# Kernel tuning notes

Hardware: AMD Instinct MI355X
Metric: run time of the kernel (lower is better)

Reference implementation:

```python
import jax, jax.numpy as jnp
import numpy as np

N, F_IN, H1, NHEADS, H2, H3 = 4096, 512, 128, 4, 256, 64
ALPHA = 0.2
NEG = -9e15


def setup_inputs() -> dict:
    key = jax.random.key(0)
    k_x, k_adj, k_watt, k_a, k_w1, k_w2 = jax.random.split(key, 6)
    x = jax.random.normal(k_x, (N, F_IN), dtype=jnp.float32)
    adj = (jax.random.uniform(k_adj, (N, N)) < 0.004).astype(jnp.float32)
    adj = adj.at[jnp.arange(N), jnp.arange(N)].set(1.0)
    # xavier-ish init scales
    W_att = jax.random.normal(k_watt, (NHEADS, F_IN, H1), dtype=jnp.float32) * (1.0 / np.sqrt(F_IN))
    a = jax.random.normal(k_a, (NHEADS, 2 * H1), dtype=jnp.float32) * 0.1
    W1 = jax.random.normal(k_w1, (NHEADS * H1, H2), dtype=jnp.float32) * (1.0 / np.sqrt(NHEADS * H1))
    W2 = jax.random.normal(k_w2, (H2, H3), dtype=jnp.float32) * (1.0 / np.sqrt(H2))
    return {"x": x, "adj": adj, "W_att": W_att, "a": a, "W1": W1, "W2": W2}


def reference(x, adj, W_att, a, W1, W2):
    h1 = W_att.shape[-1]
    # --- multi-head GAT (dense masked attention, faithful to source) ---
    Wh = jnp.einsum('nf,hfo->hno', x, W_att)              # [H, N, h1]
    a1, a2 = a[:, :h1], a[:, h1:]                          # each [H, h1]
    s1 = jnp.einsum('hno,ho->hn', Wh, a1)                  # [H, N]
    s2 = jnp.einsum('hno,ho->hn', Wh, a2)                  # [H, N]
    e = jax.nn.leaky_relu(s1[:, :, None] + s2[:, None, :], ALPHA)  # [H, N, N]
    att = jax.nn.softmax(jnp.where(adj[None] > 0, e, NEG), axis=-1)
    h = jnp.einsum('hnm,hmo->hno', att, Wh)                # [H, N, h1]
    xcat = jnp.transpose(h, (1, 0, 2)).reshape(x.shape[0], -1)  # [N, H*h1]
    xr = jax.nn.relu(xcat)
    # --- GCN layers: support = x @ W; out = adj @ support ---
    g1 = jax.nn.relu(adj @ (xr @ W1))                      # [N, H2]
    g2 = adj @ (g1 @ W2)                                   # [N, H3]
    return g2, jax.nn.softmax(g2, axis=1)
```

## Files before the change

kernel.cpp:

```cpp
#include <hip/hip_runtime.h>
#include <hip/hip_bf16.h>

#define NN    4096
#define FIN   512
#define NH1   128
#define NH    4
#define NH2   256
#define NH3   64
#define CAP   64
#define ALPHA 0.2f

typedef float f32x4 __attribute__((ext_vector_type(4)));
typedef __bf16 bf16x8 __attribute__((ext_vector_type(8)));

__device__ __forceinline__ unsigned short f2bf(float f) {
    union { float f; unsigned u; } x; x.f = f;
    unsigned r = x.u + 0x7fff + ((x.u >> 16) & 1);
    return (unsigned short)(r >> 16);
}
__device__ __forceinline__ float bf2f(ushort u) {
    union { unsigned u; float f; } x; x.u = ((unsigned)u) << 16;
    return x.f;
}
__device__ __forceinline__ float bflo(unsigned w) {
    union { unsigned u; float f; } x; x.u = w << 16; return x.f;
}
__device__ __forceinline__ float bfhi(unsigned w) {
    union { unsigned u; float f; } x; x.u = w & 0xffff0000u; return x.f;
}

#define C_X     2048
#define C_WATT  (C_X + 1024)
#define C_W1T   (C_WATT + 512)
#define C_W2B   (C_W1T + 16)
#define C_Z     (C_W2B + 32)

__global__ __launch_bounds__(256) void k_conv(
    const float* __restrict__ x, ushort* __restrict__ xb,
    const float* __restrict__ W_att, ushort* __restrict__ Wattb,
    const float* __restrict__ W1, ushort* __restrict__ W1t,
    const float* __restrict__ W2, ushort* __restrict__ W2b,
    float* __restrict__ s1s2) {
    int bid = blockIdx.x;
    int tid = threadIdx.x;
    if (bid < C_X) {
        int i = (bid * 256 + tid) * 4;
        float4 v = *reinterpret_cast<const float4*>(x + i);
        ushort4 o;
        o.x = f2bf(v.x); o.y = f2bf(v.y); o.z = f2bf(v.z); o.w = f2bf(v.w);
        *reinterpret_cast<ushort4*>(xb + i) = o;
    } else if (bid < C_WATT) {
        int idx = (bid - C_X) * 256 + tid;
        int col = idx >> 9, f = idx & 511;
        int h = col >> 7, o = col & 127;
        Wattb[idx] = f2bf(W_att[h * (FIN * NH1) + f * NH1 + o]);
    } else if (bid < C_W1T) {
        int idx = (bid - C_WATT) * 256 + tid;
        int c = idx >> 9, r = idx & 511;
        W1t[idx] = f2bf(W1[(size_t)r * NH2 + c]);
    } else if (bid < C_W2B) {
        int i = ((bid - C_W1T) * 256 + tid) * 4;
        float4 v = *reinterpret_cast<const float4*>(W2 + i);
        ushort4 o;
        o.x = f2bf(v.x); o.y = f2bf(v.y); o.z = f2bf(v.z); o.w = f2bf(v.w);
        *reinterpret_cast<ushort4*>(W2b + i) = o;
    } else {
        int i = (bid - C_W2B) * 256 + tid;
        f32x4 z = {0.f, 0.f, 0.f, 0.f};
        *reinterpret_cast<f32x4*>(s1s2 + i * 4) = z;
    }
}

#define GBM 64
#define GBN 64
#define GBK 64
template <int SCORES>
__global__ __launch_bounds__(256) void k_gemm_bf16(const ushort* __restrict__ A,
                                                   const ushort* __restrict__ Bt,
                                                   ushort* __restrict__ Cb,
                                                   const float* __restrict__ av,
                                                   float* __restrict__ s1,
                                                   float* __restrict__ s2,
                                                   int M, int N, int K) {
    __shared__ ushort As[2][GBM * GBK];
    __shared__ ushort Bs[2][GBN * GBK];
    const int tid = threadIdx.x;
    const int wid = tid >> 6;
    const int lane = tid & 63;
    const int row0 = blockIdx.y * GBM;
    const int col0 = blockIdx.x * GBN;
    const int wr = wid >> 1, wc = wid & 1;

    f32x4 acc[2][2] = {};
    const int nt = K / GBK;

    auto stage = [&](int buf, int k0) {
        #pragma unroll
        for (int j = 0; j < 2; ++j) {
            int ci = j * 256 + tid;
            int r = ci >> 3;
            int sc = (ci & 7) ^ (r & 7);
            const ushort* ga = A + (size_t)(row0 + r) * K + k0 + sc * 8;
            const ushort* gb = Bt + (size_t)(col0 + r) * K + k0 + sc * 8;
            ushort* la = &As[buf][(j * 256 + wid * 64) * 8];
            ushort* lb = &Bs[buf][(j * 256 + wid * 64) * 8];
            __builtin_amdgcn_global_load_lds(
                (const __attribute__((address_space(1))) unsigned int*)ga,
                (__attribute__((address_space(3))) unsigned int*)la, 16, 0, 0);
            __builtin_amdgcn_global_load_lds(
                (const __attribute__((address_space(1))) unsigned int*)gb,
                (__attribute__((address_space(3))) unsigned int*)lb, 16, 0, 0);
        }
    };

    stage(0, 0);
    __syncthreads();
    int cur = 0;
    for (int t = 0; t < nt; ++t) {
        if (t + 1 < nt) stage(cur ^ 1, (t + 1) * GBK);
        #pragma unroll
        for (int kk = 0; kk < 2; ++kk) {
            bf16x8 af[2], bfv[2];
            #pragma unroll
            for (int m = 0; m < 2; ++m) {
                int r = wr * 32 + m * 16 + (lane & 15);
                int kc = kk * 4 + (lane >> 4);
                int off = r * GBK + (((kc ^ (r & 7)) & 7) << 3);
                af[m] = *reinterpret_cast<const bf16x8*>(&As[cur][off]);
            }
            #pragma unroll
            for (int n = 0; n < 2; ++n) {
                int c = wc * 32 + n * 16 + (lane & 15);
                int kc = kk * 4 + (lane >> 4);
                int off = c * GBK + (((kc ^ (c & 7)) & 7) << 3);
                bfv[n] = *reinterpret_cast<const bf16x8*>(&Bs[cur][off]);
            }
            #pragma unroll
            for (int m = 0; m < 2; ++m)
                #pragma unroll
                for (int n = 0; n < 2; ++n)
                    acc[m][n] = __builtin_amdgcn_mfma_f32_16x16x32_bf16(af[m], bfv[n], acc[m][n], 0, 0, 0);
        }
        __syncthreads();
        cur ^= 1;
    }
    #pragma unroll
    for (int m = 0; m < 2; ++m)
        #pragma unroll
        for (int n = 0; n < 2; ++n) {
            int col = col0 + wc * 32 + n * 16 + (lane & 15);
            #pragma unroll
            for (int j2 = 0; j2 < 4; ++j2) {
                int row = row0 + wr * 32 + m * 16 + (lane >> 4) * 4 + j2;
                Cb[(size_t)row * N + col] = f2bf(acc[m][n][j2]);
            }
        }
    if (SCORES) {
        int h = col0 >> 7;
        float a1v[2], a2v[2];
        #pragma unroll
        for (int n = 0; n < 2; ++n) {
            int colh = (col0 & 127) + wc * 32 + n * 16 + (lane & 15);
            a1v[n] = av[h * 256 + colh];
            a2v[n] = av[h * 256 + 128 + colh];
        }
        #pragma unroll
        for (int m = 0; m < 2; ++m)
            #pragma unroll
            for (int j2 = 0; j2 < 4; ++j2) {
                float v1 = acc[m][0][j2] * a1v[0] + acc[m][1][j2] * a1v[1];
                float v2 = acc[m][0][j2] * a2v[0] + acc[m][1][j2] * a2v[1];
                #pragma unroll
                for (int off = 1; off < 16; off <<= 1) {
                    v1 += __shfl_xor(v1, off);
                    v2 += __shfl_xor(v2, off);
                }
                if ((lane & 15) == 0) {
                    int row = row0 + wr * 32 + m * 16 + (lane >> 4) * 4 + j2;
                    atomicAdd(&s1[h * NN + row], v1);
                    atomicAdd(&s2[h * NN + row], v2);
                }
            }
    }
}

__global__ __launch_bounds__(256) void k_attn_csr(const float* __restrict__ adj,
                                                  const ushort* __restrict__ Whb,
                                                  const float* __restrict__ s1,
                                                  const float* __restrict__ s2,
                                                  int* __restrict__ nbr,
                                                  int* __restrict__ cnt,
                                                  ushort* __restrict__ xrb) {
    __shared__ int lds_list[4][64];
    __shared__ int lds_cnt[4];
    __shared__ int mlist[CAP];
    __shared__ int stot;
    int n = blockIdx.x;
    int tid = threadIdx.x;
    int wid = tid >> 6;
    int lane = tid & 63;

    const uint4* arow = (const uint4*)(adj + (size_t)n * NN);
    uint4 v[4];
    #pragma unroll
    for (int it = 0; it < 4; ++it) v[it] = arow[wid * 256 + it * 64 + lane];
    const unsigned long long below = (1ull << lane) - 1ull;
    int base = 0;
    #pragma unroll
    for (int it = 0; it < 4; ++it) {
        unsigned long long b0 = __ballot(v[it].x != 0u);
        unsigned long long b1 = __ballot(v[it].y != 0u);
        unsigned long long b2 = __ballot(v[it].z != 0u);
        unsigned long long b3 = __ballot(v[it].w != 0u);
        int pre = __popcll(b0 & below) + __popcll(b1 & below) +
                  __popcll(b2 & below) + __popcll(b3 & below);
        int col0 = wid * 1024 + it * 256 + lane * 4;
        int pos = base + pre;
        if (v[it].x != 0u) { if (pos < 64) lds_list[wid][pos] = col0;     ++pos; }
        if (v[it].y != 0u) { if (pos < 64) lds_list[wid][pos] = col0 + 1; ++pos; }
        if (v[it].z != 0u) { if (pos < 64) lds_list[wid][pos] = col0 + 2; ++pos; }
        if (v[it].w != 0u) { if (pos < 64) lds_list[wid][pos] = col0 + 3; ++pos; }
        base += __popcll(b0) + __popcll(b1) + __popcll(b2) + __popcll(b3);
    }
    if (lane == 0) lds_cnt[wid] = base;
    __syncthreads();
    int c0 = lds_cnt[0], c1 = lds_cnt[1], c2 = lds_cnt[2], c3 = lds_cnt[3];
    {
        int off = (wid > 0 ? c0 : 0) + (wid > 1 ? c1 : 0) + (wid > 2 ? c2 : 0);
        int my = lds_cnt[wid]; if (my > 64) my = 64;
        if (lane < my) {
            int gpos = off + lane;
            if (gpos < CAP) {
                mlist[gpos] = lds_list[wid][lane];
                nbr[n * CAP + gpos] = lds_list[wid][lane];
            }
        }
        if (tid == 0) {
            int tot = c0 + c1 + c2 + c3;
            stot = tot < CAP ? tot : CAP;
            cnt[n] = stot;
        }
    }
    __syncthreads();
    int c = stot;

    int h = wid;
    int m = mlist[lane < c ? lane : 0];
    float e = -1e30f;
    float s1n = s1[h * NN + n];
    if (lane < c) {
        float t = s1n + s2[h * NN + m];
        e = (t >= 0.0f) ? t : ALPHA * t;
    }
    float mx = e;
    #pragma unroll
    for (int off = 32; off; off >>= 1) mx = fmaxf(mx, __shfl_xor(mx, off));
    float p = (lane < c) ? __expf(e - mx) : 0.0f;
    float s = p;
    #pragma unroll
    for (int off = 32; off; off >>= 1) s += __shfl_xor(s, off);
    p /= s;
    const ushort* wb = Whb + h * 128 + 2 * lane;
    float acc0 = 0.0f, acc1 = 0.0f;
    int cp4 = (c + 3) & ~3;
    for (int j = 0; j < cp4; j += 4) {
        float p0 = __shfl(p, j),     p1 = __shfl(p, j + 1);
        float p2 = __shfl(p, j + 2), p3 = __shfl(p, j + 3);
        int   m0 = __shfl(m, j),     m1 = __shfl(m, j + 1);
        int   m2 = __shfl(m, j + 2), m3 = __shfl(m, j + 3);
        unsigned w0 = *reinterpret_cast<const unsigned*>(wb + (size_t)m0 * 512);
        unsigned w1 = *reinterpret_cast<const unsigned*>(wb + (size_t)m1 * 512);
        unsigned w2 = *reinterpret_cast<const unsigned*>(wb + (size_t)m2 * 512);
        unsigned w3 = *reinterpret_cast<const unsigned*>(wb + (size_t)m3 * 512);
        acc0 = fmaf(p0, bflo(w0), acc0); acc1 = fmaf(p0, bfhi(w0), acc1);
        acc0 = fmaf(p1, bflo(w1), acc0); acc1 = fmaf(p1, bfhi(w1), acc1);
        acc0 = fmaf(p2, bflo(w2), acc0); acc1 = fmaf(p2, bfhi(w2), acc1);
        acc0 = fmaf(p3, bflo(w3), acc0); acc1 = fmaf(p3, bfhi(w3), acc1);
    }
    unsigned ow = (unsigned)f2bf(fmaxf(acc0, 0.0f)) | ((unsigned)f2bf(fmaxf(acc1, 0.0f)) << 16);
    *reinterpret_cast<unsigned*>(xrb + (size_t)n * 512 + h * 128 + 2 * lane) = ow;
}

__global__ __launch_bounds__(256) void k_g1y2(const ushort* __restrict__ y1b,
                                              const int* __restrict__ nbr,
                                              const int* __restrict__ cnt,
                                              const ushort* __restrict__ W2b,
                                              float* __restrict__ y2) {
    __shared__ float g1s[NH2];
    __shared__ float part[4][NH3];
    int n = blockIdx.x;
    int tid = threadIdx.x;
    int c = cnt[n];
    const int* nb = nbr + n * CAP;
    if (tid < 128) {
        float acc0 = 0.0f, acc1 = 0.0f;
        const ushort* yb = y1b + 2 * tid;
        for (int j = 0; j < c; j += 4) {
            int i0 = nb[j];
            int i1 = nb[(j + 1 < c) ? j + 1 : j];
            int i2 = nb[(j + 2 < c) ? j + 2 : j];
            int i3 = nb[(j + 3 < c) ? j + 3 : j];
            float f1 = (j + 1 < c) ? 1.f : 0.f;
            float f2 = (j + 2 < c) ? 1.f : 0.f;
            float f3 = (j + 3 < c) ? 1.f : 0.f;
            unsigned w0 = *reinterpret_cast<const unsigned*>(yb + (size_t)i0 * NH2);
            unsigned w1 = *reinterpret_cast<const unsigned*>(yb + (size_t)i1 * NH2);
            unsigned w2 = *reinterpret_cast<const unsigned*>(yb + (size_t)i2 * NH2);
            unsigned w3 = *reinterpret_cast<const unsigned*>(yb + (size_t)i3 * NH2);
            acc0 += bflo(w0); acc1 += bfhi(w0);
            acc0 = fmaf(f1, bflo(w1), acc0); acc1 = fmaf(f1, bfhi(w1), acc1);
            acc0 = fmaf(f2, bflo(w2), acc0); acc1 = fmaf(f2, bfhi(w2), acc1);
            acc0 = fmaf(f3, bflo(w3), acc0); acc1 = fmaf(f3, bfhi(w3), acc1);
        }
        g1s[2 * tid]     = fmaxf(acc0, 0.0f);
        g1s[2 * tid + 1] = fmaxf(acc1, 0.0f);
    }
    __syncthreads();
    int q = tid >> 6, col = tid & 63;
    float acc = 0.0f;
    #pragma unroll 8
    for (int i = 0; i < 64; ++i) {
        int k = q * 64 + i;
        acc = fmaf(g1s[k], bf2f(W2b[k * NH3 + col]), acc);
    }
    part[q][col] = acc;
    __syncthreads();
    if (tid < 64)
        y2[(size_t)n * NH3 + tid] = part[0][tid] + part[1][tid] + part[2][tid] + part[3][tid];
}

__global__ void k_final(const float* __restrict__ Y2, const int* __restrict__ nbr,
                        const int* __restrict__ cnt, float* __restrict__ out) {
    int n = blockIdx.x;
    int lane = threadIdx.x;
    int c = cnt[n];
    const int* nb = nbr + n * CAP;
    float acc = 0.0f;
    for (int j = 0; j < c; j += 4) {
        int i0 = nb[j];
        int i1 = nb[(j + 1 < c) ? j + 1 : j];
        int i2 = nb[(j + 2 < c) ? j + 2 : j];
        int i3 = nb[(j + 3 < c) ? j + 3 : j];
        float f1 = (j + 1 < c) ? 1.f : 0.f;
        float f2 = (j + 2 < c) ? 1.f : 0.f;
        float f3 = (j + 3 < c) ? 1.f : 0.f;
        float v0 = Y2[(size_t)i0 * NH3 + lane];
        float v1 = Y2[(size_t)i1 * NH3 + lane];
        float v2 = Y2[(size_t)i2 * NH3 + lane];
        float v3 = Y2[(size_t)i3 * NH3 + lane];
        acc += v0;
        acc = fmaf(f1, v1, acc);
        acc = fmaf(f2, v2, acc);
        acc = fmaf(f3, v3, acc);
    }
    out[(size_t)n * NH3 + lane] = acc;
    float mx = acc;
    #pragma unroll
    for (int off = 32; off; off >>= 1) mx = fmaxf(mx, __shfl_xor(mx, off));
    float p = __expf(acc - mx);
    float s = p;
    #pragma unroll
    for (int off = 32; off; off >>= 1) s += __shfl_xor(s, off);
    out[(size_t)NN * NH3 + (size_t)n * NH3 + lane] = p / s;
}

extern "C" void kernel_launch(void* const* d_in, const int* in_sizes, int n_in,
                              void* d_out, int out_size, void* d_ws, size_t ws_size,
                              hipStream_t stream) {
    const float* x     = (const float*)d_in[0];
    const float* adj   = (const float*)d_in[1];
    const float* W_att = (const float*)d_in[2];
    const float* a     = (const float*)d_in[3];
    const float* W1    = (const float*)d_in[4];
    const float* W2    = (const float*)d_in[5];
    float* out = (float*)d_out;

    char* p = (char*)d_ws;
    ushort* xb    = (ushort*)p; p += (size_t)NN * FIN * 2;
    ushort* Wattb = (ushort*)p; p += (size_t)FIN * NH * NH1 * 2;
    ushort* W1t   = (ushort*)p; p += (size_t)NH2 * (NH * NH1) * 2;
    ushort* W2b   = (ushort*)p; p += (size_t)NH2 * NH3 * 2;
    ushort* Whb   = (ushort*)p; p += (size_t)NN * NH * NH1 * 2;
    float*  s1    = (float*)p;  p += (size_t)NH * NN * 4;
    float*  s2    = (float*)p;  p += (size_t)NH * NN * 4;
    int*    nbr   = (int*)p;    p += (size_t)NN * CAP * 4;
    int*    cnt   = (int*)p;    p += (size_t)NN * 4;
    ushort* xrb   = (ushort*)p; p += (size_t)NN * NH * NH1 * 2;
    ushort* y1b   = (ushort*)p; p += (size_t)NN * NH2 * 2;
    float*  y2    = (float*)p;  p += (size_t)NN * NH3 * 4;

    k_conv<<<C_Z, 256, 0, stream>>>(x, xb, W_att, Wattb, W1, W1t, W2, W2b, s1);
    k_gemm_bf16<1><<<dim3((NH * NH1) / GBN, NN / GBM), 256, 0, stream>>>(
        xb, Wattb, Whb, a, s1, s2, NN, NH * NH1, FIN);
    k_attn_csr<<<NN, 256, 0, stream>>>(adj, Whb, s1, s2, nbr, cnt, xrb);
    k_gemm_bf16<0><<<dim3(NH2 / GBN, NN / GBM), 256, 0, stream>>>(
        xrb, W1t, y1b, nullptr, nullptr, nullptr, NN, NH2, NH * NH1);
    k_g1y2<<<NN, 256, 0, stream>>>(y1b, nbr, cnt, W2b, y2);
    k_final<<<NN, 64, 0, stream>>>(y2, nbr, cnt, out);
}
```

Measured before the change: 70.73 us.

## Template GEMM row tile, unroll gather loops by eight, pack four rows per final block

Result: faster. 67.50 us (-4.6%).

```diff
diff --git a/kernel.cpp b/kernel.cpp
--- a/kernel.cpp
+++ b/kernel.cpp
@@ -71,42 +71,45 @@
     }
 }
 
-#define GBM 64
-#define GBN 64
-#define GBK 64
-template <int SCORES>
-__global__ __launch_bounds__(256) void k_gemm_bf16(const ushort* __restrict__ A,
-                                                   const ushort* __restrict__ Bt,
-                                                   ushort* __restrict__ Cb,
-                                                   const float* __restrict__ av,
-                                                   float* __restrict__ s1,
-                                                   float* __restrict__ s2,
-                                                   int M, int N, int K) {
-    __shared__ ushort As[2][GBM * GBK];
-    __shared__ ushort Bs[2][GBN * GBK];
+template <int SCORES, int MT>
+__global__ __launch_bounds__(256) void k_gemm(const ushort* __restrict__ A,
+                                              const ushort* __restrict__ Bt,
+                                              ushort* __restrict__ Cb,
+                                              const float* __restrict__ av,
+                                              float* __restrict__ s1,
+                                              float* __restrict__ s2,
+                                              int M, int N, int K) {
+    __shared__ ushort As[2][32 * MT * 64];
+    __shared__ ushort Bs[2][64 * 64];
     const int tid = threadIdx.x;
     const int wid = tid >> 6;
     const int lane = tid & 63;
-    const int row0 = blockIdx.y * GBM;
-    const int col0 = blockIdx.x * GBN;
+    const int row0 = blockIdx.y * (32 * MT);
+    const int col0 = blockIdx.x * 64;
     const int wr = wid >> 1, wc = wid & 1;
 
-    f32x4 acc[2][2] = {};
-    const int nt = K / GBK;
+    f32x4 acc[MT][2] = {};
+    const int nt = K / 64;
 
     auto stage = [&](int buf, int k0) {
+        #pragma unroll
+        for (int j = 0; j < MT; ++j) {
+            int ci = j * 256 + tid;
+            int r = ci >> 3;
+            int sc = (ci & 7) ^ (r & 7);
+            const ushort* ga = A + (size_t)(row0 + r) * K + k0 + sc * 8;
+            ushort* la = &As[buf][(size_t)ci * 8];
+            __builtin_amdgcn_global_load_lds(
+                (const __attribute__((address_space(1))) unsigned int*)ga,
+                (__attribute__((address_space(3))) unsigned int*)la, 16, 0, 0);
+        }
         #pragma unroll
         for (int j = 0; j < 2; ++j) {
             int ci = j * 256 + tid;
             int r = ci >> 3;
             int sc = (ci & 7) ^ (r & 7);
-            const ushort* ga = A + (size_t)(row0 + r) * K + k0 + sc * 8;
             const ushort* gb = Bt + (size_t)(col0 + r) * K + k0 + sc * 8;
-            ushort* la = &As[buf][(j * 256 + wid * 64) * 8];
-            ushort* lb = &Bs[buf][(j * 256 + wid * 64) * 8];
-            __builtin_amdgcn_global_load_lds(
-                (const __attribute__((address_space(1))) unsigned int*)ga,
-                (__attribute__((address_space(3))) unsigned int*)la, 16, 0, 0);
+            ushort* lb = &Bs[buf][(size_t)ci * 8];
             __builtin_amdgcn_global_load_lds(
                 (const __attribute__((address_space(1))) unsigned int*)gb,
                 (__attribute__((address_space(3))) unsigned int*)lb, 16, 0, 0);
@@ -117,26 +120,26 @@
     __syncthreads();
     int cur = 0;
     for (int t = 0; t < nt; ++t) {
-        if (t + 1 < nt) stage(cur ^ 1, (t + 1) * GBK);
+        if (t + 1 < nt) stage(cur ^ 1, (t + 1) * 64);
         #pragma unroll
         for (int kk = 0; kk < 2; ++kk) {
-            bf16x8 af[2], bfv[2];
-            #pragma unroll
-            for (int m = 0; m < 2; ++m) {
-                int r = wr * 32 + m * 16 + (lane & 15);
+            bf16x8 af[MT], bfv[2];
+            #pragma unroll
+            for (int m = 0; m < MT; ++m) {
+                int r = wr * (16 * MT) + m * 16 + (lane & 15);
                 int kc = kk * 4 + (lane >> 4);
-                int off = r * GBK + (((kc ^ (r & 7)) & 7) << 3);
+                int off = r * 64 + (((kc ^ (r & 7)) & 7) << 3);
                 af[m] = *reinterpret_cast<const bf16x8*>(&As[cur][off]);
             }
             #pragma unroll
             for (int n = 0; n < 2; ++n) {
                 int c = wc * 32 + n * 16 + (lane & 15);
                 int kc = kk * 4 + (lane >> 4);
-                int off = c * GBK + (((kc ^ (c & 7)) & 7) << 3);
+                int off = c * 64 + (((kc ^ (c & 7)) & 7) << 3);
                 bfv[n] = *reinterpret_cast<const bf16x8*>(&Bs[cur][off]);
             }
             #pragma unroll
-            for (int m = 0; m < 2; ++m)
+            for (int m = 0; m < MT; ++m)
                 #pragma unroll
                 for (int n = 0; n < 2; ++n)
                     acc[m][n] = __builtin_amdgcn_mfma_f32_16x16x32_bf16(af[m], bfv[n], acc[m][n], 0, 0, 0);
@@ -145,13 +148,13 @@
         cur ^= 1;
     }
     #pragma unroll
-    for (int m = 0; m < 2; ++m)
+    for (int m = 0; m < MT; ++m)
         #pragma unroll
         for (int n = 0; n < 2; ++n) {
             int col = col0 + wc * 32 + n * 16 + (lane & 15);
             #pragma unroll
             for (int j2 = 0; j2 < 4; ++j2) {
-                int row = row0 + wr * 32 + m * 16 + (lane >> 4) * 4 + j2;
+                int row = row0 + wr * (16 * MT) + m * 16 + (lane >> 4) * 4 + j2;
                 Cb[(size_t)row * N + col] = f2bf(acc[m][n][j2]);
             }
         }
@@ -165,7 +168,7 @@
             a2v[n] = av[h * 256 + 128 + colh];
         }
         #pragma unroll
-        for (int m = 0; m < 2; ++m)
+        for (int m = 0; m < MT; ++m)
             #pragma unroll
             for (int j2 = 0; j2 < 4; ++j2) {
                 float v1 = acc[m][0][j2] * a1v[0] + acc[m][1][j2] * a1v[1];
@@ -176,7 +179,7 @@
                     v2 += __shfl_xor(v2, off);
                 }
                 if ((lane & 15) == 0) {
-                    int row = row0 + wr * 32 + m * 16 + (lane >> 4) * 4 + j2;
+                    int row = row0 + wr * (16 * MT) + m * 16 + (lane >> 4) * 4 + j2;
                     atomicAdd(&s1[h * NN + row], v1);
                     atomicAdd(&s2[h * NN + row], v2);
                 }
@@ -262,20 +265,22 @@
     p /= s;
     const ushort* wb = Whb + h * 128 + 2 * lane;
     float acc0 = 0.0f, acc1 = 0.0f;
-    int cp4 = (c + 3) & ~3;
-    for (int j = 0; j < cp4; j += 4) {
-        float p0 = __shfl(p, j),     p1 = __shfl(p, j + 1);
-        float p2 = __shfl(p, j + 2), p3 = __shfl(p, j + 3);
-        int   m0 = __shfl(m, j),     m1 = __shfl(m, j + 1);
-        int   m2 = __shfl(m, j + 2), m3 = __shfl(m, j + 3);
-        unsigned w0 = *reinterpret_cast<const unsigned*>(wb + (size_t)m0 * 512);
-        unsigned w1 = *reinterpret_cast<const unsigned*>(wb + (size_t)m1 * 512);
-        unsigned w2 = *reinterpret_cast<const unsigned*>(wb + (size_t)m2 * 512);
-        unsigned w3 = *reinterpret_cast<const unsigned*>(wb + (size_t)m3 * 512);
-        acc0 = fmaf(p0, bflo(w0), acc0); acc1 = fmaf(p0, bfhi(w0), acc1);
-        acc0 = fmaf(p1, bflo(w1), acc0); acc1 = fmaf(p1, bfhi(w1), acc1);
-        acc0 = fmaf(p2, bflo(w2), acc0); acc1 = fmaf(p2, bfhi(w2), acc1);
-        acc0 = fmaf(p3, bflo(w3), acc0); acc1 = fmaf(p3, bfhi(w3), acc1);
+    int cp8 = (c + 7) & ~7;
+    for (int j = 0; j < cp8; j += 8) {
+        float pj[8]; int mj[8]; unsigned wj[8];
+        #pragma unroll
+        for (int u = 0; u < 8; ++u) {
+            pj[u] = __shfl(p, j + u);
+            mj[u] = __shfl(m, j + u);
+        }
+        #pragma unroll
+        for (int u = 0; u < 8; ++u)
+            wj[u] = *reinterpret_cast<const unsigned*>(wb + (size_t)mj[u] * 512);
+        #pragma unroll
+        for (int u = 0; u < 8; ++u) {
+            acc0 = fmaf(pj[u], bflo(wj[u]), acc0);
+            acc1 = fmaf(pj[u], bfhi(wj[u]), acc1);
+        }
     }
     unsigned ow = (unsigned)f2bf(fmaxf(acc0, 0.0f)) | ((unsigned)f2bf(fmaxf(acc1, 0.0f)) << 16);
     *reinterpret_cast<unsigned*>(xrb + (size_t)n * 512 + h * 128 + 2 * lane) = ow;
@@ -295,22 +300,21 @@
     if (tid < 128) {
         float acc0 = 0.0f, acc1 = 0.0f;
         const ushort* yb = y1b + 2 * tid;
-        for (int j = 0; j < c; j += 4) {
-            int i0 = nb[j];
-            int i1 = nb[(j + 1 < c) ? j + 1 : j];
-            int i2 = nb[(j + 2 < c) ? j + 2 : j];
-            int i3 = nb[(j + 3 < c) ? j + 3 : j];
-            float f1 = (j + 1 < c) ? 1.f : 0.f;
-            float f2 = (j + 2 < c) ? 1.f : 0.f;
-            float f3 = (j + 3 < c) ? 1.f : 0.f;
-            unsigned w0 = *reinterpret_cast<const unsigned*>(yb + (size_t)i0 * NH2);
-            unsigned w1 = *reinterpret_cast<const unsigned*>(yb + (size_t)i1 * NH2);
-            unsigned w2 = *reinterpret_cast<const unsigned*>(yb + (size_t)i2 * NH2);
-            unsigned w3 = *reinterpret_cast<const unsigned*>(yb + (size_t)i3 * NH2);
-            acc0 += bflo(w0); acc1 += bfhi(w0);
-            acc0 = fmaf(f1, bflo(w1), acc0); acc1 = fmaf(f1, bfhi(w1), acc1);
-            acc0 = fmaf(f2, bflo(w2), acc0); acc1 = fmaf(f2, bfhi(w2), acc1);
-            acc0 = fmaf(f3, bflo(w3), acc0); acc1 = fmaf(f3, bfhi(w3), acc1);
+        for (int j = 0; j < c; j += 8) {
+            int idx[8]; float f[8]; unsigned w[8];
+            #pragma unroll
+            for (int u = 0; u < 8; ++u) {
+                idx[u] = nb[(j + u < c) ? j + u : j];
+                f[u] = (j + u < c) ? 1.f : 0.f;
+            }
+            #pragma unroll
+            for (int u = 0; u < 8; ++u)
+                w[u] = *reinterpret_cast<const unsigned*>(yb + (size_t)idx[u] * NH2);
+            #pragma unroll
+            for (int u = 0; u < 8; ++u) {
+                acc0 = fmaf(f[u], bflo(w[u]), acc0);
+                acc1 = fmaf(f[u], bfhi(w[u]), acc1);
+            }
         }
         g1s[2 * tid]     = fmaxf(acc0, 0.0f);
         g1s[2 * tid + 1] = fmaxf(acc1, 0.0f);
@@ -329,29 +333,28 @@
         y2[(size_t)n * NH3 + tid] = part[0][tid] + part[1][tid] + part[2][tid] + part[3][tid];
 }
 
-__global__ void k_final(const float* __restrict__ Y2, const int* __restrict__ nbr,
-                        const int* __restrict__ cnt, float* __restrict__ out) {
-    int n = blockIdx.x;
-    int lane = threadIdx.x;
+__global__ __launch_bounds__(256) void k_final(const float* __restrict__ Y2,
+                                               const int* __restrict__ nbr,
+                                               const int* __restrict__ cnt,
+                                               float* __restrict__ out) {
+    int n = blockIdx.x * 4 + (threadIdx.x >> 6);
+    int lane = threadIdx.x & 63;
     int c = cnt[n];
     const int* nb = nbr + n * CAP;
     float acc = 0.0f;
-    for (int j = 0; j < c; j += 4) {
-        int i0 = nb[j];
-        int i1 = nb[(j + 1 < c) ? j + 1 : j];
-        int i2 = nb[(j + 2 < c) ? j + 2 : j];
-        int i3 = nb[(j + 3 < c) ? j + 3 : j];
-        float f1 = (j + 1 < c) ? 1.f : 0.f;
-        float f2 = (j + 2 < c) ? 1.f : 0.f;
-        float f3 = (j + 3 < c) ? 1.f : 0.f;
-        float v0 = Y2[(size_t)i0 * NH3 + lane];
-        float v1 = Y2[(size_t)i1 * NH3 + lane];
-        float v2 = Y2[(size_t)i2 * NH3 + lane];
-        float v3 = Y2[(size_t)i3 * NH3 + lane];
-        acc += v0;
-        acc = fmaf(f1, v1, acc);
-        acc = fmaf(f2, v2, acc);
-        acc = fmaf(f3, v3, acc);
+    for (int j = 0; j < c; j += 8) {
+        int idx[8]; float f[8]; float v[8];
+        #pragma unroll
+        for (int u = 0; u < 8; ++u) {
+            idx[u] = nb[(j + u < c) ? j + u : j];
+            f[u] = (j + u < c) ? 1.f : 0.f;
+        }
+        #pragma unroll
+        for (int u = 0; u < 8; ++u)
+            v[u] = Y2[(size_t)idx[u] * NH3 + lane];
+        #pragma unroll
+        for (int u = 0; u < 8; ++u)
+            acc = fmaf(f[u], v[u], acc);
     }
     out[(size_t)n * NH3 + lane] = acc;
     float mx = acc;
@@ -390,11 +393,11 @@
     float*  y2    = (float*)p;  p += (size_t)NN * NH3 * 4;
 
     k_conv<<<C_Z, 256, 0, stream>>>(x, xb, W_att, Wattb, W1, W1t, W2, W2b, s1);
-    k_gemm_bf16<1><<<dim3((NH * NH1) / GBN, NN / GBM), 256, 0, stream>>>(
+    k_gemm<1, 2><<<dim3((NH * NH1) / 64, NN / 64), 256, 0, stream>>>(
         xb, Wattb, Whb, a, s1, s2, NN, NH * NH1, FIN);
     k_attn_csr<<<NN, 256, 0, stream>>>(adj, Whb, s1, s2, nbr, cnt, xrb);
-    k_gemm_bf16<0><<<dim3(NH2 / GBN, NN / GBM), 256, 0, stream>>>(
+    k_gemm<0, 1><<<dim3(NH2 / 64, NN / 32), 256, 0, stream>>>(
         xrb, W1t, y1b, nullptr, nullptr, nullptr, NN, NH2, NH * NH1);
     k_g1y2<<<NN, 256, 0, stream>>>(y1b, nbr, cnt, W2b, y2);
-    k_final<<<NN, 64, 0, stream>>>(y2, nbr, cnt, out);
-}
+    k_final<<<NN / 4, 256, 0, stream>>>(y2, nbr, cnt, out);
+}
```
